# Optimization experiments

Measured on AMD Instinct MI355X. Metric: run time of the kernel, lower is better.

Reference implementation:

```python
import jax, jax.numpy as jnp
import numpy as np

B, P, K = 8, 1024, 20  # clouds, points per cloud, kNN neighbors
OUT = 40
EPS = 1e-5


def leaky(x):
    return jnp.where(x >= 0, x, 0.2 * x)


def batch_norm(h, gamma, beta):
    mu = jnp.mean(h, axis=0)
    var = jnp.var(h, axis=0)
    return (h - mu) * jax.lax.rsqrt(var + EPS) * gamma + beta


def edge_conv(x, W, b, k):
    # x: [B,P,C]. Dynamic kNN in feature space (self included, as torch_cluster knn),
    # edge feature nn([x_i, x_j - x_i]) (single plain Linear per PyG MLP plain_last),
    # then max-aggregation over the k neighbors.
    sq = jnp.sum(x * x, axis=-1)                                  # [B,P]
    d = sq[:, :, None] + sq[:, None, :] - 2.0 * jnp.einsum('bpc,bqc->bpq', x, x)
    idx = jax.lax.top_k(-d, k)[1]                                  # [B,P,k]
    xj = jax.vmap(lambda xc, ic: xc[ic])(x, idx)                   # [B,P,k,C]
    xi = jnp.broadcast_to(x[:, :, None, :], xj.shape)
    e = jnp.concatenate([xi, xj - xi], axis=-1)                    # [B,P,k,2C]
    h = jnp.einsum('bpke,ec->bpkc', e, W) + b
    return jnp.max(h, axis=2)                                      # [B,P,Cout]


def setup_inputs() -> dict:
    key = jax.random.key(0)
    ks = jax.random.split(key, 16)
    s = 0.1
    pos = jax.random.normal(ks[0], (B * P, 3), dtype=jnp.float32)
    batch = jnp.repeat(jnp.arange(B, dtype=jnp.int32), P)
    return {
        'pos': pos, 'batch': batch,
        'W1': jax.random.normal(ks[1], (6, 64), jnp.float32) * s,    'b1': jnp.zeros((64,), jnp.float32),
        'W2': jax.random.normal(ks[2], (128, 64), jnp.float32) * s,  'b2': jnp.zeros((64,), jnp.float32),
        'W3': jax.random.normal(ks[3], (128, 128), jnp.float32) * s, 'b3': jnp.zeros((128,), jnp.float32),
        'W4': jax.random.normal(ks[4], (256, 256), jnp.float32) * s, 'b4': jnp.zeros((256,), jnp.float32),
        'Wm': jax.random.normal(ks[5], (512, 1024), jnp.float32) * s, 'bm': jnp.zeros((1024,), jnp.float32),
        'Wa': jax.random.normal(ks[6], (2048, 512), jnp.float32) * s, 'ba': jnp.zeros((512,), jnp.float32),
        'ga': jnp.ones((512,), jnp.float32),  'bea': jnp.zeros((512,), jnp.float32),
        'Wb': jax.random.normal(ks[7], (512, 256), jnp.float32) * s, 'bb': jnp.zeros((256,), jnp.float32),
        'gb': jnp.ones((256,), jnp.float32),  'beb': jnp.zeros((256,), jnp.float32),
        'Wc': jax.random.normal(ks[8], (256, OUT), jnp.float32) * s, 'bc': jnp.zeros((OUT,), jnp.float32),
    }


def reference(pos, batch, W1, b1, W2, b2, W3, b3, W4, b4, Wm, bm,
              Wa, ba, ga, bea, Wb, bb, gb, beb, Wc, bc):
    # batch ids are contiguous with P points per cloud -> reshape to [B,P,.]
    x = pos.reshape(B, P, 3)
    x1 = edge_conv(x, W1, b1, K)    # [B,P,64]
    x2 = edge_conv(x1, W2, b2, K)   # [B,P,64]
    x3 = edge_conv(x2, W3, b3, K)   # [B,P,128]
    x4 = edge_conv(x3, W4, b4, K)   # [B,P,256]
    cat = jnp.concatenate([x1, x2, x3, x4], axis=-1)  # [B,P,512]
    out = cat @ Wm + bm                                # [B,P,1024] (plain Linear)
    gmax = jnp.max(out, axis=1)                        # global_max_pool  [B,1024]
    gmean = jnp.mean(out, axis=1)                      # global_mean_pool [B,1024]
    h = jnp.concatenate([gmax, gmean], axis=-1)        # [B,2048]
    h = leaky(batch_norm(h @ Wa + ba, ga, bea))        # dropout = identity (eval)
    h = leaky(batch_norm(h @ Wb + bb, gb, beb))
    return h @ Wc + bc                                 # [B,40]
```

## Files before the change

kernel.cpp:

```cpp
#include <hip/hip_runtime.h>
#include <hip/hip_bf16.h>

#define NB 8
#define NP 1024
#define NPTS (NB * NP)
#define KNN 20

using bf16x8 = __attribute__((ext_vector_type(8))) short;
using f32x4 = __attribute__((ext_vector_type(4))) float;

static __device__ __forceinline__ unsigned long long umin64(unsigned long long a,
                                                            unsigned long long b) {
    return a < b ? a : b;
}

static __device__ __forceinline__ void split_bf16(float v, unsigned short& h,
                                                  unsigned short& l) {
    __hip_bfloat16 hb = __float2bfloat16(v);
    float hf = __bfloat162float(hb);
    __hip_bfloat16 lb = __float2bfloat16(v - hf);
    h = *(unsigned short*)&hb;
    l = *(unsigned short*)&lb;
}

static __device__ __forceinline__ unsigned long long wave_bitonic_sort(
        unsigned long long v, int lane) {
#pragma unroll
    for (int k = 2; k <= 64; k <<= 1) {
#pragma unroll
        for (int j = k >> 1; j > 0; j >>= 1) {
            unsigned long long o = __shfl_xor(v, j, 64);
            bool tmin = (((lane & k) == 0) == ((lane & j) == 0));
            bool lt = v < o;
            v = (lt == tmin) ? v : o;
        }
    }
    return v;
}

static __device__ __forceinline__ void topk20_wave(unsigned long long k[16], int lane,
                                                   int* __restrict__ out) {
    for (int r = 0; r < KNN; ++r) {
        unsigned long long m = k[0];
#pragma unroll
        for (int j = 1; j < 16; ++j)
            if ((unsigned)(k[j] >> 32) < (unsigned)(m >> 32)) m = k[j];
#pragma unroll
        for (int s = 1; s < 64; s <<= 1) {
            unsigned long long o = __shfl_xor(m, s, 64);
            m = umin64(m, o);
        }
        if (lane == 0) out[r] = (int)(m & 0xffffffffu);
        if (r == KNN - 1) break;
        unsigned mlo = (unsigned)m;
#pragma unroll
        for (int j = 0; j < 16; ++j)
            if ((unsigned)k[j] == mlo) k[j] = ~0ull;
    }
}

static __device__ __forceinline__ void topk20_fast(unsigned long long k[16], int lane,
                                                   unsigned long long* __restrict__ cand,
                                                   int* __restrict__ out) {
    unsigned long long lm = k[0];
#pragma unroll
    for (int j = 1; j < 16; ++j) lm = umin64(lm, k[j]);
    unsigned long long s = wave_bitonic_sort(lm, lane);
    unsigned long long T = __shfl(s, 19, 64);

    int base = 0;
#pragma unroll
    for (int j = 0; j < 16; ++j) {
        bool sel = (k[j] <= T);
        unsigned long long mask = __ballot(sel);
        if (sel) {
            int pos = base + (int)__popcll(mask & ((1ull << lane) - 1ull));
            if (pos < 64) cand[pos] = k[j];
        }
        base += (int)__popcll(mask);
    }
    if (base <= 64) {
        unsigned long long v = (lane < base) ? cand[lane] : ~0ull;
        v = wave_bitonic_sort(v, lane);
        if (lane < KNN) out[lane] = (int)(v & 0xffffffffu);
    } else {
        topk20_wave(k, lane, out);
    }
}

__global__ __launch_bounds__(256) void knn3_kernel(const float* __restrict__ x,
                                                   int* __restrict__ idx) {
    const int w = threadIdx.x >> 6, lane = threadIdx.x & 63;
    const int p = blockIdx.x * 4 + w;
    const int b = p >> 10, pr = p & 1023;
    const int tid = threadIdx.x;
    __shared__ float sx[3][1024];
    __shared__ float ssq[1024];
    __shared__ unsigned long long cand[4][64];
    const float* xb = x + (size_t)b * NP * 3;

    for (int t = tid; t < 1024; t += 256) {
        float vx = xb[t * 3 + 0], vy = xb[t * 3 + 1], vz = xb[t * 3 + 2];
        sx[0][t] = vx;
        sx[1][t] = vy;
        sx[2][t] = vz;
        ssq[t] = vx * vx + vy * vy + vz * vz;
    }
    __syncthreads();

    const float px = sx[0][pr], py = sx[1][pr], pz = sx[2][pr];
    const float sqp = ssq[pr];

    unsigned long long k[16];
#pragma unroll
    for (int j = 0; j < 16; ++j) {
        int q = j * 64 + lane;
        float dot = px * sx[0][q];
        dot += py * sx[1][q];
        dot += pz * sx[2][q];
        float d = sqp + ssq[q] - 2.0f * dot;
        unsigned u = __float_as_uint(d);
        u = (u & 0x80000000u) ? ~u : (u | 0x80000000u);
        k[j] = ((unsigned long long)u << 32) | (unsigned)q;
    }
    topk20_fast(k, lane, cand[w], idx + (size_t)p * KNN);
}

template <int C>
__global__ __launch_bounds__(256) void sqnorm_kernel(const float* __restrict__ x,
                                                     float* __restrict__ sqn) {
    int p = blockIdx.x * 256 + threadIdx.x;
    if (p < NPTS) {
        const float* xp = x + (size_t)p * C;
        float s = 0.f;
        for (int c = 0; c < C; ++c) s += xp[c] * xp[c];
        sqn[p] = s;
    }
}

template <int C>
__global__ __launch_bounds__(256) void convert_x_kernel(const float* __restrict__ x,
                                                        unsigned short* __restrict__ Xh,
                                                        unsigned short* __restrict__ Xl) {
    int g = blockIdx.x * 256 + threadIdx.x;
    int p = g & (NPTS - 1), ks = g >> 13;
    const float* src = x + (size_t)p * C + ks * 8;
    float4 v0 = ((const float4*)src)[0];
    float4 v1 = ((const float4*)src)[1];
    float v[8] = {v0.x, v0.y, v0.z, v0.w, v1.x, v1.y, v1.z, v1.w};
    unsigned short h[8], l[8];
#pragma unroll
    for (int j = 0; j < 8; ++j) split_bf16(v[j], h[j], l[j]);
    size_t ci = (size_t)ks * NPTS + p;
    uint4 hp, lp;
    hp.x = h[0] | ((unsigned)h[1] << 16);
    hp.y = h[2] | ((unsigned)h[3] << 16);
    hp.z = h[4] | ((unsigned)h[5] << 16);
    hp.w = h[6] | ((unsigned)h[7] << 16);
    lp.x = l[0] | ((unsigned)l[1] << 16);
    lp.y = l[2] | ((unsigned)l[3] << 16);
    lp.z = l[4] | ((unsigned)l[5] << 16);
    lp.w = l[6] | ((unsigned)l[7] << 16);
    ((uint4*)Xh)[ci] = hp;
    ((uint4*)Xl)[ci] = lp;
}

template <int Cin, int Cout>
__global__ __launch_bounds__(256) void convert_w_edge_kernel(
        const float* __restrict__ W, unsigned short* __restrict__ Wh,
        unsigned short* __restrict__ Wl) {
    constexpr int N2 = 2 * Cout;
    int g = blockIdx.x * 256 + threadIdx.x;
    if (g >= (Cin / 8) * N2) return;
    int n = g % N2, ks = g / N2;
    unsigned short h[8], l[8];
#pragma unroll
    for (int j = 0; j < 8; ++j) {
        int c = ks * 8 + j;
        float v;
        if (n < Cout)
            v = W[(size_t)c * Cout + n] - W[(size_t)(Cin + c) * Cout + n];
        else
            v = W[(size_t)(Cin + c) * Cout + (n - Cout)];
        split_bf16(v, h[j], l[j]);
    }
    size_t ci = (size_t)ks * N2 + n;
    uint4 hp, lp;
    hp.x = h[0] | ((unsigned)h[1] << 16);
    hp.y = h[2] | ((unsigned)h[3] << 16);
    hp.z = h[4] | ((unsigned)h[5] << 16);
    hp.w = h[6] | ((unsigned)h[7] << 16);
    lp.x = l[0] | ((unsigned)l[1] << 16);
    lp.y = l[2] | ((unsigned)l[3] << 16);
    lp.z = l[4] | ((unsigned)l[5] << 16);
    lp.w = l[6] | ((unsigned)l[7] << 16);
    ((uint4*)Wh)[ci] = hp;
    ((uint4*)Wl)[ci] = lp;
}

template <int C>
__global__ __launch_bounds__(256, 2) void dist_mfma_kernel(
        const unsigned short* __restrict__ Xhp, const unsigned short* __restrict__ Xlp,
        const float* __restrict__ sqn, float* __restrict__ Dm) {
    constexpr int NCK = C / 32;
    const int b = blockIdx.z;
    const int p0 = blockIdx.y * 128;
    const int q0 = blockIdx.x * 128;
    const int g0 = b * NP;
    const int tid = threadIdx.x;
    const int wid = tid >> 6, lane = tid & 63;
    const int wm = (wid >> 1) * 64, wn = (wid & 1) * 64;

    __shared__ uint4 sAh[2][4][132], sAl[2][4][132], sBh[2][4][132], sBl[2][4][132];
    __shared__ float sqa[128], sqb[128];

    f32x4 acc[4][4];
#pragma unroll
    for (int i = 0; i < 4; ++i)
#pragma unroll
        for (int j = 0; j < 4; ++j) acc[i][j] = {0.f, 0.f, 0.f, 0.f};

    const uint4* Ah4 = (const uint4*)Xhp;
    const uint4* Al4 = (const uint4*)Xlp;

    const int m0 = tid & 127, kb0 = tid >> 7;
    uint4 rAh0, rAl0, rBh0, rBl0, rAh1, rAl1, rBh1, rBl1;

#define DM_LOAD(ck)                                                     \
    {                                                                   \
        int ksb = (ck) * 4;                                             \
        size_t a0 = (size_t)(ksb + kb0) * NPTS + g0 + p0 + m0;          \
        size_t a1 = (size_t)(ksb + kb0 + 2) * NPTS + g0 + p0 + m0;      \
        size_t b0 = (size_t)(ksb + kb0) * NPTS + g0 + q0 + m0;          \
        size_t b1 = (size_t)(ksb + kb0 + 2) * NPTS + g0 + q0 + m0;      \
        rAh0 = Ah4[a0]; rAl0 = Al4[a0];                                 \
        rAh1 = Ah4[a1]; rAl1 = Al4[a1];                                 \
        rBh0 = Ah4[b0]; rBl0 = Al4[b0];                                 \
        rBh1 = Ah4[b1]; rBl1 = Al4[b1];                                 \
    }

#define DM_WRITE(buf)                                                   \
    {                                                                   \
        sAh[buf][kb0][m0] = rAh0;  sAl[buf][kb0][m0] = rAl0;            \
        sAh[buf][kb0 + 2][m0] = rAh1;  sAl[buf][kb0 + 2][m0] = rAl1;    \
        sBh[buf][kb0][m0] = rBh0;  sBl[buf][kb0][m0] = rBl0;            \
        sBh[buf][kb0 + 2][m0] = rBh1;  sBl[buf][kb0 + 2][m0] = rBl1;    \
    }

    DM_LOAD(0);
    DM_WRITE(0);
    __syncthreads();

    const int fkb = lane >> 4, flm = lane & 15;

    for (int ck = 0; ck < NCK; ++ck) {
        const int buf = ck & 1;
        if (ck < NCK - 1) DM_LOAD(ck + 1);

        bf16x8 fAh[4], fAl[4], fBh[4], fBl[4];
#pragma unroll
        for (int i = 0; i < 4; ++i) {
            fAh[i] = *(const bf16x8*)&sAh[buf][fkb][wm + i * 16 + flm];
            fAl[i] = *(const bf16x8*)&sAl[buf][fkb][wm + i * 16 + flm];
            fBh[i] = *(const bf16x8*)&sBh[buf][fkb][wn + i * 16 + flm];
            fBl[i] = *(const bf16x8*)&sBl[buf][fkb][wn + i * 16 + flm];
        }
#pragma unroll
        for (int i = 0; i < 4; ++i)
#pragma unroll
            for (int j = 0; j < 4; ++j) {
                acc[i][j] = __builtin_amdgcn_mfma_f32_16x16x32_bf16(fAh[i], fBh[j],
                                                                    acc[i][j], 0, 0, 0);
                acc[i][j] = __builtin_amdgcn_mfma_f32_16x16x32_bf16(fAh[i], fBl[j],
                                                                    acc[i][j], 0, 0, 0);
                acc[i][j] = __builtin_amdgcn_mfma_f32_16x16x32_bf16(fAl[i], fBh[j],
                                                                    acc[i][j], 0, 0, 0);
            }

        if (ck < NCK - 1) DM_WRITE(buf ^ 1);
        __syncthreads();
    }

    if (tid < 128) sqa[tid] = sqn[g0 + p0 + tid];
    else sqb[tid - 128] = sqn[g0 + q0 + (tid - 128)];
    __syncthreads();

    const int r4 = (lane >> 4) * 4, cc = lane & 15;
#pragma unroll
    for (int i = 0; i < 4; ++i) {
#pragma unroll
        for (int r = 0; r < 4; ++r) {
            int row = wm + i * 16 + r4 + r;
            float sp = sqa[row];
            float* drow = Dm + ((size_t)(g0 + p0 + row)) * NP + q0;
#pragma unroll
            for (int j = 0; j < 4; ++j) {
                int col = wn + j * 16 + cc;
                drow[col] = sp + sqb[col] - 2.0f * acc[i][j][r];
            }
        }
    }
#undef DM_LOAD
#undef DM_WRITE
}

template <int Cin, int Cout>
__global__ __launch_bounds__(256, 2) void edge_mfma_kernel(
        const unsigned short* __restrict__ Xhp, const unsigned short* __restrict__ Xlp,
        const unsigned short* __restrict__ Whp, const unsigned short* __restrict__ Wlp,
        const float* __restrict__ bias, float* __restrict__ AB) {
    constexpr int N2 = 2 * Cout;
    constexpr int NCK = Cin / 32;
    const int n0 = blockIdx.x * 128;
    const int p0 = blockIdx.y * 128;
    const int tid = threadIdx.x;
    const int wid = tid >> 6, lane = tid & 63;
    const int wm = (wid >> 1) * 64, wn = (wid & 1) * 64;

    __shared__ uint4 sAh[2][4][132], sAl[2][4][132], sBh[2][4][132], sBl[2][4][132];

    f32x4 acc[4][4];
#pragma unroll
    for (int i = 0; i < 4; ++i)
#pragma unroll
        for (int j = 0; j < 4; ++j) acc[i][j] = {0.f, 0.f, 0.f, 0.f};

    const uint4* Ah4 = (const uint4*)Xhp;
    const uint4* Al4 = (const uint4*)Xlp;
    const uint4* Wh4 = (const uint4*)Whp;
    const uint4* Wl4 = (const uint4*)Wlp;

    const int m0 = tid & 127, kb0 = tid >> 7;
    uint4 rAh0, rAl0, rBh0, rBl0, rAh1, rAl1, rBh1, rBl1;

#define EM_LOAD(ck)                                                     \
    {                                                                   \
        int ksb = (ck) * 4;                                             \
        size_t a0 = (size_t)(ksb + kb0) * NPTS + p0 + m0;               \
        size_t a1 = (size_t)(ksb + kb0 + 2) * NPTS + p0 + m0;           \
        size_t b0 = (size_t)(ksb + kb0) * N2 + n0 + m0;                 \
        size_t b1 = (size_t)(ksb + kb0 + 2) * N2 + n0 + m0;             \
        rAh0 = Ah4[a0]; rAl0 = Al4[a0];                                 \
        rAh1 = Ah4[a1]; rAl1 = Al4[a1];                                 \
        rBh0 = Wh4[b0]; rBl0 = Wl4[b0];                                 \
        rBh1 = Wh4[b1]; rBl1 = Wl4[b1];                                 \
    }

#define EM_WRITE(buf)                                                   \
    {                                                                   \
        sAh[buf][kb0][m0] = rAh0;  sAl[buf][kb0][m0] = rAl0;            \
        sAh[buf][kb0 + 2][m0] = rAh1;  sAl[buf][kb0 + 2][m0] = rAl1;    \
        sBh[buf][kb0][m0] = rBh0;  sBl[buf][kb0][m0] = rBl0;            \
        sBh[buf][kb0 + 2][m0] = rBh1;  sBl[buf][kb0 + 2][m0] = rBl1;    \
    }

    EM_LOAD(0);
    EM_WRITE(0);
    __syncthreads();

    const int fkb = lane >> 4, flm = lane & 15;

    for (int ck = 0; ck < NCK; ++ck) {
        const int buf = ck & 1;
        if (ck < NCK - 1) EM_LOAD(ck + 1);

        bf16x8 fAh[4], fAl[4], fBh[4], fBl[4];
#pragma unroll
        for (int i = 0; i < 4; ++i) {
            fAh[i] = *(const bf16x8*)&sAh[buf][fkb][wm + i * 16 + flm];
            fAl[i] = *(const bf16x8*)&sAl[buf][fkb][wm + i * 16 + flm];
            fBh[i] = *(const bf16x8*)&sBh[buf][fkb][wn + i * 16 + flm];
            fBl[i] = *(const bf16x8*)&sBl[buf][fkb][wn + i * 16 + flm];
        }
#pragma unroll
        for (int i = 0; i < 4; ++i)
#pragma unroll
            for (int j = 0; j < 4; ++j) {
                acc[i][j] = __builtin_amdgcn_mfma_f32_16x16x32_bf16(fAh[i], fBh[j],
                                                                    acc[i][j], 0, 0, 0);
                acc[i][j] = __builtin_amdgcn_mfma_f32_16x16x32_bf16(fAh[i], fBl[j],
                                                                    acc[i][j], 0, 0, 0);
                acc[i][j] = __builtin_amdgcn_mfma_f32_16x16x32_bf16(fAl[i], fBh[j],
                                                                    acc[i][j], 0, 0, 0);
            }

        if (ck < NCK - 1) EM_WRITE(buf ^ 1);
        __syncthreads();
    }

    const int r4 = (lane >> 4) * 4, cc = lane & 15;
    float bj[4];
#pragma unroll
    for (int j = 0; j < 4; ++j) {
        int cg = n0 + wn + j * 16 + cc;
        bj[j] = (cg < Cout) ? bias[cg] : 0.f;
    }
#pragma unroll
    for (int i = 0; i < 4; ++i) {
#pragma unroll
        for (int r = 0; r < 4; ++r) {
            int row = wm + i * 16 + r4 + r;
            float* orow = AB + (size_t)(p0 + row) * N2 + n0;
#pragma unroll
            for (int j = 0; j < 4; ++j)
                orow[wn + j * 16 + cc] = acc[i][j][r] + bj[j];
        }
    }
#undef EM_LOAD
#undef EM_WRITE
}

__global__ __launch_bounds__(256) void topk_kernel(const float* __restrict__ Dm,
                                                   int* __restrict__ idx) {
    const int w = threadIdx.x >> 6, lane = threadIdx.x & 63;
    const int p = blockIdx.x * 4 + w;
    const int b = p >> 10, pr = p & 1023;
    const float* row = Dm + ((size_t)b * NP + pr) * NP;
    __shared__ unsigned long long cand[4][64];

    unsigned long long k[16];
#pragma unroll
    for (int j = 0; j < 16; ++j) {
        int q = j * 64 + lane;
        float dv = row[q];
        unsigned u = __float_as_uint(dv);
        u = (u & 0x80000000u) ? ~u : (u | 0x80000000u);
        k[j] = ((unsigned long long)u << 32) | (unsigned)q;
    }
    topk20_fast(k, lane, cand[w], idx + (size_t)p * KNN);
}

template <int Cin, int Cout>
__global__ __launch_bounds__(256) void edge_gemm_kernel(const float* __restrict__ x,
                                                        const float* __restrict__ W,
                                                        const float* __restrict__ bias,
                                                        float* __restrict__ AB) {
    constexpr int N2 = 2 * Cout;
    constexpr int BK = (Cin < 32) ? Cin : 32;
    const int n0 = blockIdx.x * 128;
    const int p0 = blockIdx.y * 64;
    const int tid = threadIdx.x;
    const int tx = tid & 15, ty = tid >> 4;

    __shared__ float sX[BK][68];
    __shared__ float sW[BK][132];

    float acc[4][8];
#pragma unroll
    for (int i = 0; i < 4; ++i)
#pragma unroll
        for (int j = 0; j < 8; ++j) acc[i][j] = 0.f;

    for (int k0 = 0; k0 < Cin; k0 += BK) {
        for (int t = tid; t < 64 * BK; t += 256) {
            int m = t / BK, c = t - m * BK;
            sX[c][m] = x[(size_t)(p0 + m) * Cin + c];
        }
        for (int t = tid; t < BK * 128; t += 256) {
            int c = t >> 7, n = t & 127;
            int nn = n0 + n;
            float w;
            if (nn < Cout)
                w = W[(size_t)(k0 + c) * Cout + nn] - W[(size_t)(Cin + k0 + c) * Cout + nn];
            else
                w = W[(size_t)(Cin + k0 + c) * Cout + (nn - Cout)];
            sW[c][n] = w;
        }
        __syncthreads();

#pragma unroll
        for (int c = 0; c < BK; ++c) {
            float4 a4 = *(const float4*)&sX[c][ty * 4];
            float4 w0 = *(const float4*)&sW[c][tx * 4];
            float4 w1 = *(const float4*)&sW[c][64 + tx * 4];
            float av[4] = {a4.x, a4.y, a4.z, a4.w};
#pragma unroll
            for (int i = 0; i < 4; ++i) {
                acc[i][0] += av[i] * w0.x;
                acc[i][1] += av[i] * w0.y;
                acc[i][2] += av[i] * w0.z;
                acc[i][3] += av[i] * w0.w;
                acc[i][4] += av[i] * w1.x;
                acc[i][5] += av[i] * w1.y;
                acc[i][6] += av[i] * w1.z;
                acc[i][7] += av[i] * w1.w;
            }
        }
        __syncthreads();
    }

    const bool aH0 = (n0 < Cout);
    const bool aH1 = (n0 + 64 < Cout);
    float4 z4 = {0.f, 0.f, 0.f, 0.f};
    float4 bb0 = aH0 ? *(const float4*)&bias[n0 + tx * 4] : z4;
    float4 bb1 = aH1 ? *(const float4*)&bias[n0 + 64 + tx * 4] : z4;

#pragma unroll
    for (int i = 0; i < 4; ++i) {
        float* orow = AB + (size_t)(p0 + ty * 4 + i) * N2 + n0;
        float4 o0, o1;
        o0.x = acc[i][0] + bb0.x;
        o0.y = acc[i][1] + bb0.y;
        o0.z = acc[i][2] + bb0.z;
        o0.w = acc[i][3] + bb0.w;
        o1.x = acc[i][4] + bb1.x;
        o1.y = acc[i][5] + bb1.y;
        o1.z = acc[i][6] + bb1.z;
        o1.w = acc[i][7] + bb1.w;
        *(float4*)&orow[tx * 4] = o0;
        *(float4*)&orow[64 + tx * 4] = o1;
    }
}

template <int Cout>
__global__ __launch_bounds__(256) void gather_max_kernel(const float* __restrict__ AB,
                                                         const int* __restrict__ idx,
                                                         float* __restrict__ y) {
    constexpr int N2 = 2 * Cout;
    constexpr int TPP = Cout / 4;
    constexpr int PPB = 256 / TPP;
    constexpr int RS = N2 / 4;
    const int pp = threadIdx.x / TPP;
    const int t = threadIdx.x % TPP;
    const int p = blockIdx.x * PPB + pp;
    const int base = p & ~(NP - 1);

    __shared__ int s_idx[PPB][KNN];
    for (int tt = threadIdx.x; tt < PPB * KNN; tt += 256) {
        int a = tt / KNN, r = tt - a * KNN;
        s_idx[a][r] = idx[(size_t)(blockIdx.x * PPB + a) * KNN + r];
    }
    __syncthreads();

    const float4* Brow = (const float4*)(AB + (size_t)base * N2 + Cout);

    int q0 = s_idx[pp][0];
    float4 m = Brow[(size_t)q0 * RS + t];
#pragma unroll
    for (int j = 1; j < KNN; ++j) {
        int q = s_idx[pp][j];
        float4 v = Brow[(size_t)q * RS + t];
        m.x = fmaxf(m.x, v.x);
        m.y = fmaxf(m.y, v.y);
        m.z = fmaxf(m.z, v.z);
        m.w = fmaxf(m.w, v.w);
    }
    float4 a = *(const float4*)(AB + (size_t)p * N2 + 4 * t);
    float4 o;
    o.x = a.x + m.x;
    o.y = a.y + m.y;
    o.z = a.z + m.z;
    o.w = a.w + m.w;
    *(float4*)(y + (size_t)p * Cout + 4 * t) = o;
}

__global__ __launch_bounds__(256) void convert_w_kernel(const float* __restrict__ Wm,
                                                        unsigned short* __restrict__ Wh,
                                                        unsigned short* __restrict__ Wl) {
    int g = blockIdx.x * 256 + threadIdx.x;
    int n = g & 1023, ks = g >> 10;
    unsigned short h[8], l[8];
#pragma unroll
    for (int j = 0; j < 8; ++j) {
        float v = Wm[(size_t)(ks * 8 + j) * 1024 + n];
        split_bf16(v, h[j], l[j]);
    }
    size_t ci = (size_t)ks * 1024 + n;
    uint4 hp, lp;
    hp.x = h[0] | ((unsigned)h[1] << 16);
    hp.y = h[2] | ((unsigned)h[3] << 16);
    hp.z = h[4] | ((unsigned)h[5] << 16);
    hp.w = h[6] | ((unsigned)h[7] << 16);
    lp.x = l[0] | ((unsigned)l[1] << 16);
    lp.y = l[2] | ((unsigned)l[3] << 16);
    lp.z = l[4] | ((unsigned)l[5] << 16);
    lp.w = l[6] | ((unsigned)l[7] << 16);
    ((uint4*)Wh)[ci] = hp;
    ((uint4*)Wl)[ci] = lp;
}

__global__ __launch_bounds__(256) void catmean_kernel(
        const float* __restrict__ x1, const float* __restrict__ x2,
        const float* __restrict__ x3, const float* __restrict__ x4,
        float* __restrict__ catmean) {
    const int n0 = blockIdx.x * 128;
    const int b = blockIdx.y;
    const int tid = threadIdx.x;
    const int col = n0 + (tid & 127);
    const int half = tid >> 7;
    __shared__ float sred[256];

    const float* src;
    int cw, coff;
    if (col < 64) { src = x1; cw = 64; coff = col; }
    else if (col < 128) { src = x2; cw = 64; coff = col - 64; }
    else if (col < 256) { src = x3; cw = 128; coff = col - 128; }
    else { src = x4; cw = 256; coff = col - 256; }

    float s = 0.f;
    const float* base = src + ((size_t)b * NP + half * 512) * cw + coff;
    for (int p = 0; p < 512; ++p) s += base[(size_t)p * cw];
    sred[tid] = s;
    __syncthreads();
    if (tid < 128)
        catmean[(size_t)b * 512 + col] = (sred[tid] + sred[tid + 128]) * (1.0f / 1024.0f);
}

__global__ __launch_bounds__(256) void gmean_kernel(const float* __restrict__ catmean,
                                                    const float* __restrict__ Wm,
                                                    const float* __restrict__ bm,
                                                    float* __restrict__ gmeanv) {
    const int n0 = blockIdx.x * 128;
    const int b = blockIdx.y;
    const int tid = threadIdx.x;
    const int cg = tid & 31, kp = tid >> 5;
    const int col = n0 + cg * 4;
    __shared__ float4 part[8][32];

    float4 acc = {0.f, 0.f, 0.f, 0.f};
    for (int k = kp * 64; k < kp * 64 + 64; ++k) {
        float g = catmean[(size_t)b * 512 + k];
        float4 w = *(const float4*)&Wm[(size_t)k * 1024 + col];
        acc.x += g * w.x;
        acc.y += g * w.y;
        acc.z += g * w.z;
        acc.w += g * w.w;
    }
    part[kp][cg] = acc;
    __syncthreads();
    if (tid < 32) {
        float4 s = part[0][tid];
#pragma unroll
        for (int z = 1; z < 8; ++z) {
            float4 p = part[z][tid];
            s.x += p.x; s.y += p.y; s.z += p.z; s.w += p.w;
        }
        float4 bb = *(const float4*)&bm[n0 + tid * 4];
        s.x += bb.x; s.y += bb.y; s.z += bb.z; s.w += bb.w;
        *(float4*)&gmeanv[(size_t)b * 1024 + n0 + tid * 4] = s;
    }
}

__global__ __launch_bounds__(256, 2) void gemm_cat_pool_kernel(
        const unsigned short* __restrict__ Ahp, const unsigned short* __restrict__ Alp,
        const unsigned short* __restrict__ Whp, const unsigned short* __restrict__ Wlp,
        float* __restrict__ pmax) {
    const int bid = blockIdx.x;
    const int xcd = bid & 7, pos = bid >> 3;
    const int nb = pos & 7, pb = (xcd << 3) | (pos >> 3);
    const int n0 = nb * 128, p0 = pb * 128;
    const int tid = threadIdx.x;
    const int wid = tid >> 6, lane = tid & 63;
    const int wm = (wid >> 1) * 64, wn = (wid & 1) * 64;

    __shared__ uint4 sAh[2][4][132], sAl[2][4][132], sBh[2][4][132], sBl[2][4][132];
    __shared__ float sMax[2][128];

    f32x4 acc[4][4];
#pragma unroll
    for (int i = 0; i < 4; ++i)
#pragma unroll
        for (int j = 0; j < 4; ++j) acc[i][j] = {0.f, 0.f, 0.f, 0.f};

    const uint4* Ah4 = (const uint4*)Ahp;
    const uint4* Al4 = (const uint4*)Alp;
    const uint4* Wh4 = (const uint4*)Whp;
    const uint4* Wl4 = (const uint4*)Wlp;

    const int m0 = tid & 127, kb0 = tid >> 7;
    uint4 rAh0, rAl0, rBh0, rBl0, rAh1, rAl1, rBh1, rBl1;

#define MP_LOAD(ck)                                                     \
    {                                                                   \
        int ksb = (ck) * 4;                                             \
        size_t a0 = (size_t)(ksb + kb0) * 8192 + p0 + m0;               \
        size_t a1 = (size_t)(ksb + kb0 + 2) * 8192 + p0 + m0;           \
        size_t b0 = (size_t)(ksb + kb0) * 1024 + n0 + m0;               \
        size_t b1 = (size_t)(ksb + kb0 + 2) * 1024 + n0 + m0;           \
        rAh0 = Ah4[a0]; rAl0 = Al4[a0];                                 \
        rAh1 = Ah4[a1]; rAl1 = Al4[a1];                                 \
        rBh0 = Wh4[b0]; rBl0 = Wl4[b0];                                 \
        rBh1 = Wh4[b1]; rBl1 = Wl4[b1];                                 \
    }

#define MP_WRITE(buf)                                                   \
    {                                                                   \
        sAh[buf][kb0][m0] = rAh0;  sAl[buf][kb0][m0] = rAl0;            \
        sAh[buf][kb0 + 2][m0] = rAh1;  sAl[buf][kb0 + 2][m0] = rAl1;    \
        sBh[buf][kb0][m0] = rBh0;  sBl[buf][kb0][m0] = rBl0;            \
        sBh[buf][kb0 + 2][m0] = rBh1;  sBl[buf][kb0 + 2][m0] = rBl1;    \
    }

    MP_LOAD(0);
    MP_WRITE(0);
    __syncthreads();

    const int fkb = lane >> 4, flm = lane & 15;

    for (int ck = 0; ck < 16; ++ck) {
        const int buf = ck & 1;
        if (ck < 15) MP_LOAD(ck + 1);

        bf16x8 fAh[4], fAl[4], fBh[4], fBl[4];
#pragma unroll
        for (int i = 0; i < 4; ++i) {
            fAh[i] = *(const bf16x8*)&sAh[buf][fkb][wm + i * 16 + flm];
            fAl[i] = *(const bf16x8*)&sAl[buf][fkb][wm + i * 16 + flm];
            fBh[i] = *(const bf16x8*)&sBh[buf][fkb][wn + i * 16 + flm];
            fBl[i] = *(const bf16x8*)&sBl[buf][fkb][wn + i * 16 + flm];
        }
#pragma unroll
        for (int i = 0; i < 4; ++i)
#pragma unroll
            for (int j = 0; j < 4; ++j) {
                acc[i][j] = __builtin_amdgcn_mfma_f32_16x16x32_bf16(fAh[i], fBh[j],
                                                                    acc[i][j], 0, 0, 0);
                acc[i][j] = __builtin_amdgcn_mfma_f32_16x16x32_bf16(fAh[i], fBl[j],
                                                                    acc[i][j], 0, 0, 0);
                acc[i][j] = __builtin_amdgcn_mfma_f32_16x16x32_bf16(fAl[i], fBh[j],
                                                                    acc[i][j], 0, 0, 0);
            }

        if (ck < 15) MP_WRITE(buf ^ 1);
        __syncthreads();
    }

    float cm[4];
#pragma unroll
    for (int j = 0; j < 4; ++j) {
        float m = acc[0][j][0];
#pragma unroll
        for (int i = 0; i < 4; ++i)
#pragma unroll
            for (int r = 0; r < 4; ++r) m = fmaxf(m, acc[i][j][r]);
        m = fmaxf(m, __shfl_xor(m, 16, 64));
        m = fmaxf(m, __shfl_xor(m, 32, 64));
        cm[j] = m;
    }
    if (lane < 16) {
#pragma unroll
        for (int j = 0; j < 4; ++j) sMax[wid >> 1][wn + j * 16 + lane] = cm[j];
    }
    __syncthreads();
    if (tid < 128)
        pmax[(size_t)pb * 1024 + n0 + tid] = fmaxf(sMax[0][tid], sMax[1][tid]);
#undef MP_LOAD
#undef MP_WRITE
}

__global__ __launch_bounds__(256) void fc_a_kernel(const float* __restrict__ pmax,
                                                   const float* __restrict__ gmeanv,
                                                   const float* __restrict__ bm,
                                                   const float* __restrict__ Wa,
                                                   const float* __restrict__ ba,
                                                   float* __restrict__ ha) {
    const int b = blockIdx.y;
    const int n0 = blockIdx.x * 64;
    const int tid = threadIdx.x;
    __shared__ float gm[2048];
    __shared__ float4 part[16][16];

    for (int c = tid; c < 1024; c += 256) {
        float m = pmax[(size_t)(b * 8) * 1024 + c];
#pragma unroll
        for (int z = 1; z < 8; ++z) m = fmaxf(m, pmax[(size_t)(b * 8 + z) * 1024 + c]);
        gm[c] = m + bm[c];
        gm[1024 + c] = gmeanv[(size_t)b * 1024 + c];
    }
    __syncthreads();

    const int cg = tid & 15, kp = tid >> 4;
    const int co = n0 + cg * 4;
    float4 acc = {0.f, 0.f, 0.f, 0.f};
    const float* Wp = Wa + (size_t)(kp * 128) * 512 + co;
    const float* gp = gm + kp * 128;
#pragma unroll 8
    for (int k = 0; k < 128; ++k) {
        float g = gp[k];
        float4 w = *(const float4*)&Wp[(size_t)k * 512];
        acc.x += g * w.x;
        acc.y += g * w.y;
        acc.z += g * w.z;
        acc.w += g * w.w;
    }
    part[kp][cg] = acc;
    __syncthreads();
    if (tid < 16) {
        float4 s = part[0][tid];
#pragma unroll
        for (int z = 1; z < 16; ++z) {
            float4 p = part[z][tid];
            s.x += p.x; s.y += p.y; s.z += p.z; s.w += p.w;
        }
        float4 bb = *(const float4*)&ba[n0 + tid * 4];
        s.x += bb.x; s.y += bb.y; s.z += bb.z; s.w += bb.w;
        *(float4*)&ha[(size_t)b * 512 + n0 + tid * 4] = s;
    }
}

__global__ __launch_bounds__(256) void bn_leaky_kernel(float* __restrict__ h,
                                                       const float* __restrict__ g,
                                                       const float* __restrict__ be,
                                                       int ncol) {
    int co = blockIdx.x * 256 + threadIdx.x;
    if (co >= ncol) return;
    float mu = 0.f;
    for (int b = 0; b < NB; ++b) mu += h[b * ncol + co];
    mu *= 0.125f;
    float var = 0.f;
    for (int b = 0; b < NB; ++b) {
        float d = h[b * ncol + co] - mu;
        var += d * d;
    }
    var *= 0.125f;
    float inv = 1.0f / sqrtf(var + 1e-5f);
    for (int b = 0; b < NB; ++b) {
        float v = (h[b * ncol + co] - mu) * inv * g[co] + be[co];
        h[b * ncol + co] = v >= 0.f ? v : 0.2f * v;
    }
}

__global__ __launch_bounds__(256) void fc_b_kernel(const float* __restrict__ ha,
                                                   const float* __restrict__ Wb,
                                                   const float* __restrict__ bb,
                                                   float* __restrict__ hb) {
    const int b = blockIdx.y;
    const int n0 = blockIdx.x * 64;
    const int tid = threadIdx.x;
    __shared__ float sh[512];
    __shared__ float4 part[16][16];

    for (int c = tid; c < 512; c += 256) sh[c] = ha[(size_t)b * 512 + c];
    __syncthreads();

    const int cg = tid & 15, kp = tid >> 4;
    const int co = n0 + cg * 4;
    float4 acc = {0.f, 0.f, 0.f, 0.f};
#pragma unroll 8
    for (int k = 0; k < 32; ++k) {
        float g = sh[kp * 32 + k];
        float4 w = *(const float4*)&Wb[(size_t)(kp * 32 + k) * 256 + co];
        acc.x += g * w.x;
        acc.y += g * w.y;
        acc.z += g * w.z;
        acc.w += g * w.w;
    }
    part[kp][cg] = acc;
    __syncthreads();
    if (tid < 16) {
        float4 s = part[0][tid];
#pragma unroll
        for (int z = 1; z < 16; ++z) {
            float4 p = part[z][tid];
            s.x += p.x; s.y += p.y; s.z += p.z; s.w += p.w;
        }
        float4 bv = *(const float4*)&bb[n0 + tid * 4];
        s.x += bv.x; s.y += bv.y; s.z += bv.z; s.w += bv.w;
        *(float4*)&hb[(size_t)b * 256 + n0 + tid * 4] = s;
    }
}

__global__ __launch_bounds__(256) void fc_c_kernel(const float* __restrict__ hb,
                                                   const float* __restrict__ Wc,
                                                   const float* __restrict__ bc,
                                                   float* __restrict__ outp) {
    int t = blockIdx.x * 256 + threadIdx.x;
    if (t >= 8 * 40) return;
    int b = t / 40, o = t - b * 40;
    float s = bc[o];
    for (int c = 0; c < 256; ++c) s += hb[b * 256 + c] * Wc[c * 40 + o];
    outp[t] = s;
}

extern "C" void kernel_launch(void* const* d_in, const int* in_sizes, int n_in,
                              void* d_out, int out_size, void* d_ws, size_t ws_size,
                              hipStream_t stream) {
    const float* pos = (const float*)d_in[0];
    const float* W1 = (const float*)d_in[2];
    const float* b1 = (const float*)d_in[3];
    const float* W2 = (const float*)d_in[4];
    const float* b2 = (const float*)d_in[5];
    const float* W3 = (const float*)d_in[6];
    const float* b3 = (const float*)d_in[7];
    const float* W4 = (const float*)d_in[8];
    const float* b4 = (const float*)d_in[9];
    const float* Wm = (const float*)d_in[10];
    const float* bm = (const float*)d_in[11];
    const float* Wa = (const float*)d_in[12];
    const float* ba = (const float*)d_in[13];
    const float* ga = (const float*)d_in[14];
    const float* bea = (const float*)d_in[15];
    const float* Wb = (const float*)d_in[16];
    const float* bb = (const float*)d_in[17];
    const float* gb = (const float*)d_in[18];
    const float* beb = (const float*)d_in[19];
    const float* Wc = (const float*)d_in[20];
    const float* bc = (const float*)d_in[21];
    float* out = (float*)d_out;

    char* ws = (char*)d_ws;
    size_t off = 0;
    auto alloc = [&](size_t bytes) {
        void* p = ws + off;
        off += (bytes + 255) & ~(size_t)255;
        return p;
    };
    int* idx = (int*)alloc((size_t)NPTS * KNN * 4);
    float* x1 = (float*)alloc((size_t)NPTS * 64 * 4);
    float* x2 = (float*)alloc((size_t)NPTS * 64 * 4);
    float* x3 = (float*)alloc((size_t)NPTS * 128 * 4);
    float* x4 = (float*)alloc((size_t)NPTS * 256 * 4);
    float* scratch = (float*)alloc((size_t)NPTS * 1024 * 4);
    float* pmax = (float*)alloc((size_t)64 * 1024 * 4);
    float* catmean = (float*)alloc(NB * 512 * 4);
    float* gmeanv = (float*)alloc(NB * 1024 * 4);
    float* ha = (float*)alloc(NB * 512 * 4);
    float* hb = (float*)alloc(NB * 256 * 4);
    float* sqn = (float*)alloc(NPTS * 4);
    unsigned short* Ach = (unsigned short*)alloc((size_t)64 * NPTS * 8 * 2);
    unsigned short* Acl = (unsigned short*)alloc((size_t)64 * NPTS * 8 * 2);
    unsigned short* Wth = (unsigned short*)alloc((size_t)64 * 1024 * 8 * 2);
    unsigned short* Wtl = (unsigned short*)alloc((size_t)64 * 1024 * 8 * 2);
    unsigned short* Weh = (unsigned short*)alloc((size_t)16 * 512 * 8 * 2);
    unsigned short* Wel = (unsigned short*)alloc((size_t)16 * 512 * 8 * 2);
    (void)ws_size;

    float* Dm = scratch;
    float* AB = scratch;
    const size_t REG = (size_t)NPTS * 8;
    unsigned short* x1h = Ach, *x1l = Acl;
    unsigned short* x2h = Ach + 8 * REG, *x2l = Acl + 8 * REG;
    unsigned short* x3h = Ach + 16 * REG, *x3l = Acl + 16 * REG;
    unsigned short* x4h = Ach + 32 * REG, *x4l = Acl + 32 * REG;

    dim3 dmg(8, 8, 8);

    knn3_kernel<<<NPTS / 4, 256, 0, stream>>>(pos, idx);
    edge_gemm_kernel<3, 64><<<dim3(1, 128), 256, 0, stream>>>(pos, W1, b1, AB);
    gather_max_kernel<64><<<NPTS / 16, 256, 0, stream>>>(AB, idx, x1);

    convert_x_kernel<64><<<NPTS * 8 / 256, 256, 0, stream>>>(x1, x1h, x1l);
    sqnorm_kernel<64><<<NPTS / 256, 256, 0, stream>>>(x1, sqn);
    dist_mfma_kernel<64><<<dmg, 256, 0, stream>>>(x1h, x1l, sqn, Dm);
    topk_kernel<<<NPTS / 4, 256, 0, stream>>>(Dm, idx);
    convert_w_edge_kernel<64, 64><<<4, 256, 0, stream>>>(W2, Weh, Wel);
    edge_mfma_kernel<64, 64><<<dim3(1, 64), 256, 0, stream>>>(x1h, x1l, Weh, Wel, b2, AB);
    gather_max_kernel<64><<<NPTS / 16, 256, 0, stream>>>(AB, idx, x2);

    convert_x_kernel<64><<<NPTS * 8 / 256, 256, 0, stream>>>(x2, x2h, x2l);
    sqnorm_kernel<64><<<NPTS / 256, 256, 0, stream>>>(x2, sqn);
    dist_mfma_kernel<64><<<dmg, 256, 0, stream>>>(x2h, x2l, sqn, Dm);
    topk_kernel<<<NPTS / 4, 256, 0, stream>>>(Dm, idx);
    convert_w_edge_kernel<64, 128><<<8, 256, 0, stream>>>(W3, Weh, Wel);
    edge_mfma_kernel<64, 128><<<dim3(2, 64), 256, 0, stream>>>(x2h, x2l, Weh, Wel, b3, AB);
    gather_max_kernel<128><<<NPTS / 8, 256, 0, stream>>>(AB, idx, x3);

    convert_x_kernel<128><<<NPTS * 16 / 256, 256, 0, stream>>>(x3, x3h, x3l);
    sqnorm_kernel<128><<<NPTS / 256, 256, 0, stream>>>(x3, sqn);
    dist_mfma_kernel<128><<<dmg, 256, 0, stream>>>(x3h, x3l, sqn, Dm);
    topk_kernel<<<NPTS / 4, 256, 0, stream>>>(Dm, idx);
    convert_w_edge_kernel<128, 256><<<32, 256, 0, stream>>>(W4, Weh, Wel);
    edge_mfma_kernel<128, 256><<<dim3(4, 64), 256, 0, stream>>>(x3h, x3l, Weh, Wel, b4, AB);
    gather_max_kernel<256><<<NPTS / 4, 256, 0, stream>>>(AB, idx, x4);

    convert_x_kernel<256><<<NPTS * 32 / 256, 256, 0, stream>>>(x4, x4h, x4l);

    catmean_kernel<<<dim3(4, NB), 256, 0, stream>>>(x1, x2, x3, x4, catmean);
    gmean_kernel<<<dim3(8, NB), 256, 0, stream>>>(catmean, Wm, bm, gmeanv);

    convert_w_kernel<<<256, 256, 0, stream>>>(Wm, Wth, Wtl);

    gemm_cat_pool_kernel<<<512, 256, 0, stream>>>(Ach, Acl, Wth, Wtl, pmax);

    fc_a_kernel<<<dim3(8, NB), 256, 0, stream>>>(pmax, gmeanv, bm, Wa, ba, ha);
    bn_leaky_kernel<<<2, 256, 0, stream>>>(ha, ga, bea, 512);
    fc_b_kernel<<<dim3(4, NB), 256, 0, stream>>>(ha, Wb, bb, hb);
    bn_leaky_kernel<<<1, 256, 0, stream>>>(hb, gb, beb, 256);
    fc_c_kernel<<<2, 256, 0, stream>>>(hb, Wc, bc, out);
}
```

Baseline: 269.2 us.

## Fuse distance GEMM and top-k selection into one kNN kernel via shared memory

Replaces the separate distance-matrix MFMA kernel and top-k kernel with one fused kernel. Each block computes a 16-row slab of the 1024-column distance matrix into LDS and runs top-20 selection per row directly, so the 32 MB distance matrix never goes to global memory. The scratch buffer shrinks to match. In exchange, B operands are loaded from global without LDS staging, each block re-reads the whole cloud's features, and the large LDS footprint (~66KB) limits occupancy.

```diff
diff --git a/kernel.cpp b/kernel.cpp
--- a/kernel.cpp
+++ b/kernel.cpp
@@ -199,109 +199,95 @@
 }
 
 template <int C>
-__global__ __launch_bounds__(256, 2) void dist_mfma_kernel(
+__global__ __launch_bounds__(256, 2) void knn_mfma_kernel(
         const unsigned short* __restrict__ Xhp, const unsigned short* __restrict__ Xlp,
-        const float* __restrict__ sqn, float* __restrict__ Dm) {
+        const float* __restrict__ sqn, int* __restrict__ idx) {
     constexpr int NCK = C / 32;
-    const int b = blockIdx.z;
-    const int p0 = blockIdx.y * 128;
-    const int q0 = blockIdx.x * 128;
+    const int bid = blockIdx.x;
+    const int b = bid >> 6, rg = bid & 63;
     const int g0 = b * NP;
+    const int p0 = rg * 16;
     const int tid = threadIdx.x;
     const int wid = tid >> 6, lane = tid & 63;
-    const int wm = (wid >> 1) * 64, wn = (wid & 1) * 64;
-
-    __shared__ uint4 sAh[2][4][132], sAl[2][4][132], sBh[2][4][132], sBl[2][4][132];
-    __shared__ float sqa[128], sqb[128];
-
-    f32x4 acc[4][4];
-#pragma unroll
-    for (int i = 0; i < 4; ++i)
-#pragma unroll
-        for (int j = 0; j < 4; ++j) acc[i][j] = {0.f, 0.f, 0.f, 0.f};
+    const int fkb = lane >> 4, flm = lane & 15;
+
+    __shared__ float sD[16][1028];
+    __shared__ float sqa[16];
+    __shared__ float sqb[1024];
+    __shared__ unsigned long long cand[4][64];
+
+    if (tid < 16) sqa[tid] = sqn[g0 + p0 + tid];
+    for (int t = tid; t < 1024; t += 256) sqb[t] = sqn[g0 + t];
+    __syncthreads();
 
     const uint4* Ah4 = (const uint4*)Xhp;
     const uint4* Al4 = (const uint4*)Xlp;
 
-    const int m0 = tid & 127, kb0 = tid >> 7;
-    uint4 rAh0, rAl0, rBh0, rBl0, rAh1, rAl1, rBh1, rBl1;
-
-#define DM_LOAD(ck)                                                     \
-    {                                                                   \
-        int ksb = (ck) * 4;                                             \
-        size_t a0 = (size_t)(ksb + kb0) * NPTS + g0 + p0 + m0;          \
-        size_t a1 = (size_t)(ksb + kb0 + 2) * NPTS + g0 + p0 + m0;      \
-        size_t b0 = (size_t)(ksb + kb0) * NPTS + g0 + q0 + m0;          \
-        size_t b1 = (size_t)(ksb + kb0 + 2) * NPTS + g0 + q0 + m0;      \
-        rAh0 = Ah4[a0]; rAl0 = Al4[a0];                                 \
-        rAh1 = Ah4[a1]; rAl1 = Al4[a1];                                 \
-        rBh0 = Ah4[b0]; rBl0 = Al4[b0];                                 \
-        rBh1 = Ah4[b1]; rBl1 = Al4[b1];                                 \
-    }
-
-#define DM_WRITE(buf)                                                   \
-    {                                                                   \
-        sAh[buf][kb0][m0] = rAh0;  sAl[buf][kb0][m0] = rAl0;            \
-        sAh[buf][kb0 + 2][m0] = rAh1;  sAl[buf][kb0 + 2][m0] = rAl1;    \
-        sBh[buf][kb0][m0] = rBh0;  sBl[buf][kb0][m0] = rBl0;            \
-        sBh[buf][kb0 + 2][m0] = rBh1;  sBl[buf][kb0 + 2][m0] = rBl1;    \
-    }
-
-    DM_LOAD(0);
-    DM_WRITE(0);
-    __syncthreads();
-
-    const int fkb = lane >> 4, flm = lane & 15;
-
-    for (int ck = 0; ck < NCK; ++ck) {
-        const int buf = ck & 1;
-        if (ck < NCK - 1) DM_LOAD(ck + 1);
-
-        bf16x8 fAh[4], fAl[4], fBh[4], fBl[4];
-#pragma unroll
-        for (int i = 0; i < 4; ++i) {
-            fAh[i] = *(const bf16x8*)&sAh[buf][fkb][wm + i * 16 + flm];
-            fAl[i] = *(const bf16x8*)&sAl[buf][fkb][wm + i * 16 + flm];
-            fBh[i] = *(const bf16x8*)&sBh[buf][fkb][wn + i * 16 + flm];
-            fBl[i] = *(const bf16x8*)&sBl[buf][fkb][wn + i * 16 + flm];
-        }
-#pragma unroll
-        for (int i = 0; i < 4; ++i)
-#pragma unroll
-            for (int j = 0; j < 4; ++j) {
-                acc[i][j] = __builtin_amdgcn_mfma_f32_16x16x32_bf16(fAh[i], fBh[j],
-                                                                    acc[i][j], 0, 0, 0);
-                acc[i][j] = __builtin_amdgcn_mfma_f32_16x16x32_bf16(fAh[i], fBl[j],
-                                                                    acc[i][j], 0, 0, 0);
-                acc[i][j] = __builtin_amdgcn_mfma_f32_16x16x32_bf16(fAl[i], fBh[j],
-                                                                    acc[i][j], 0, 0, 0);
+    uint4 fAh[NCK], fAl[NCK];
+#pragma unroll
+    for (int kk = 0; kk < NCK; ++kk) {
+        size_t a = (size_t)(4 * kk + fkb) * NPTS + g0 + p0 + flm;
+        fAh[kk] = Ah4[a];
+        fAl[kk] = Al4[a];
+    }
+
+    const int r4 = fkb * 4, cc = flm;
+
+#pragma unroll
+    for (int t = 0; t < 2; ++t) {
+        const int c0 = (wid + t * 4) * 128;
+        f32x4 acc[8];
+#pragma unroll
+        for (int j = 0; j < 8; ++j) acc[j] = {0.f, 0.f, 0.f, 0.f};
+
+#pragma unroll
+        for (int kk = 0; kk < NCK; ++kk) {
+            uint4 fBh[8], fBl[8];
+#pragma unroll
+            for (int j = 0; j < 8; ++j) {
+                size_t bi = (size_t)(4 * kk + fkb) * NPTS + g0 + c0 + j * 16 + flm;
+                fBh[j] = Ah4[bi];
+                fBl[j] = Al4[bi];
             }
-
-        if (ck < NCK - 1) DM_WRITE(buf ^ 1);
-        __syncthreads();
-    }
-
-    if (tid < 128) sqa[tid] = sqn[g0 + p0 + tid];
-    else sqb[tid - 128] = sqn[g0 + q0 + (tid - 128)];
-    __syncthreads();
-
-    const int r4 = (lane >> 4) * 4, cc = lane & 15;
-#pragma unroll
-    for (int i = 0; i < 4; ++i) {
+            bf16x8 ah = *(const bf16x8*)&fAh[kk];
+            bf16x8 al = *(const bf16x8*)&fAl[kk];
+#pragma unroll
+            for (int j = 0; j < 8; ++j) {
+                bf16x8 bh = *(const bf16x8*)&fBh[j];
+                bf16x8 bl = *(const bf16x8*)&fBl[j];
+                acc[j] = __builtin_amdgcn_mfma_f32_16x16x32_bf16(ah, bh, acc[j], 0, 0, 0);
+                acc[j] = __builtin_amdgcn_mfma_f32_16x16x32_bf16(ah, bl, acc[j], 0, 0, 0);
+                acc[j] = __builtin_amdgcn_mfma_f32_16x16x32_bf16(al, bh, acc[j], 0, 0, 0);
+            }
+        }
+
 #pragma unroll
         for (int r = 0; r < 4; ++r) {
-            int row = wm + i * 16 + r4 + r;
+            int row = r4 + r;
             float sp = sqa[row];
-            float* drow = Dm + ((size_t)(g0 + p0 + row)) * NP + q0;
-#pragma unroll
-            for (int j = 0; j < 4; ++j) {
-                int col = wn + j * 16 + cc;
-                drow[col] = sp + sqb[col] - 2.0f * acc[i][j][r];
+#pragma unroll
+            for (int j = 0; j < 8; ++j) {
+                int col = c0 + j * 16 + cc;
+                sD[row][col] = sp + sqb[col] - 2.0f * acc[j][r];
             }
         }
     }
-#undef DM_LOAD
-#undef DM_WRITE
+    __syncthreads();
+
+    for (int rr = 0; rr < 4; ++rr) {
+        int row = wid * 4 + rr;
+        unsigned long long k[16];
+#pragma unroll
+        for (int j = 0; j < 16; ++j) {
+            int q = j * 64 + lane;
+            float dv = sD[row][q];
+            unsigned u = __float_as_uint(dv);
+            u = (u & 0x80000000u) ? ~u : (u | 0x80000000u);
+            k[j] = ((unsigned long long)u << 32) | (unsigned)q;
+        }
+        topk20_fast(k, lane, cand[wid], idx + (size_t)(g0 + p0 + row) * KNN);
+        __builtin_amdgcn_s_barrier();
+    }
 }
 
 template <int Cin, int Cout>
@@ -408,26 +394,6 @@
     }
 #undef EM_LOAD
 #undef EM_WRITE
-}
-
-__global__ __launch_bounds__(256) void topk_kernel(const float* __restrict__ Dm,
-                                                   int* __restrict__ idx) {
-    const int w = threadIdx.x >> 6, lane = threadIdx.x & 63;
-    const int p = blockIdx.x * 4 + w;
-    const int b = p >> 10, pr = p & 1023;
-    const float* row = Dm + ((size_t)b * NP + pr) * NP;
-    __shared__ unsigned long long cand[4][64];
-
-    unsigned long long k[16];
-#pragma unroll
-    for (int j = 0; j < 16; ++j) {
-        int q = j * 64 + lane;
-        float dv = row[q];
-        unsigned u = __float_as_uint(dv);
-        u = (u & 0x80000000u) ? ~u : (u | 0x80000000u);
-        k[j] = ((unsigned long long)u << 32) | (unsigned)q;
-    }
-    topk20_fast(k, lane, cand[w], idx + (size_t)p * KNN);
 }
 
 template <int Cin, int Cout>
@@ -910,7 +876,7 @@
     float* x2 = (float*)alloc((size_t)NPTS * 64 * 4);
     float* x3 = (float*)alloc((size_t)NPTS * 128 * 4);
     float* x4 = (float*)alloc((size_t)NPTS * 256 * 4);
-    float* scratch = (float*)alloc((size_t)NPTS * 1024 * 4);
+    float* scratch = (float*)alloc((size_t)NPTS * 512 * 4);
     float* pmax = (float*)alloc((size_t)64 * 1024 * 4);
     float* catmean = (float*)alloc(NB * 512 * 4);
     float* gmeanv = (float*)alloc(NB * 1024 * 4);
@@ -925,7 +891,6 @@
     unsigned short* Wel = (unsigned short*)alloc((size_t)16 * 512 * 8 * 2);
     (void)ws_size;
 
-    float* Dm = scratch;
     float* AB = scratch;
     const size_t REG = (size_t)NPTS * 8;
     unsigned short* x1h = Ach, *x1l = Acl;
@@ -933,32 +898,27 @@
     unsigned short* x3h = Ach + 16 * REG, *x3l = Acl + 16 * REG;
     unsigned short* x4h = Ach + 32 * REG, *x4l = Acl + 32 * REG;
 
-    dim3 dmg(8, 8, 8);
-
     knn3_kernel<<<NPTS / 4, 256, 0, stream>>>(pos, idx);
     edge_gemm_kernel<3, 64><<<dim3(1, 128), 256, 0, stream>>>(pos, W1, b1, AB);
     gather_max_kernel<64><<<NPTS / 16, 256, 0, stream>>>(AB, idx, x1);
 
     convert_x_kernel<64><<<NPTS * 8 / 256, 256, 0, stream>>>(x1, x1h, x1l);
     sqnorm_kernel<64><<<NPTS / 256, 256, 0, stream>>>(x1, sqn);
-    dist_mfma_kernel<64><<<dmg, 256, 0, stream>>>(x1h, x1l, sqn, Dm);
-    topk_kernel<<<NPTS / 4, 256, 0, stream>>>(Dm, idx);
+    knn_mfma_kernel<64><<<512, 256, 0, stream>>>(x1h, x1l, sqn, idx);
     convert_w_edge_kernel<64, 64><<<4, 256, 0, stream>>>(W2, Weh, Wel);
     edge_mfma_kernel<64, 64><<<dim3(1, 64), 256, 0, stream>>>(x1h, x1l, Weh, Wel, b2, AB);
     gather_max_kernel<64><<<NPTS / 16, 256, 0, stream>>>(AB, idx, x2);
 
     convert_x_kernel<64><<<NPTS * 8 / 256, 256, 0, stream>>>(x2, x2h, x2l);
     sqnorm_kernel<64><<<NPTS / 256, 256, 0, stream>>>(x2, sqn);
-    dist_mfma_kernel<64><<<dmg, 256, 0, stream>>>(x2h, x2l, sqn, Dm);
-    topk_kernel<<<NPTS / 4, 256, 0, stream>>>(Dm, idx);
+    knn_mfma_kernel<64><<<512, 256, 0, stream>>>(x2h, x2l, sqn, idx);
     convert_w_edge_kernel<64, 128><<<8, 256, 0, stream>>>(W3, Weh, Wel);
     edge_mfma_kernel<64, 128><<<dim3(2, 64), 256, 0, stream>>>(x2h, x2l, Weh, Wel, b3, AB);
     gather_max_kernel<128><<<NPTS / 8, 256, 0, stream>>>(AB, idx, x3);
 
     convert_x_kernel<128><<<NPTS * 16 / 256, 256, 0, stream>>>(x3, x3h, x3l);
     sqnorm_kernel<128><<<NPTS / 256, 256, 0, stream>>>(x3, sqn);
-    dist_mfma_kernel<128><<<dmg, 256, 0, stream>>>(x3h, x3l, sqn, Dm);
-    topk_kernel<<<NPTS / 4, 256, 0, stream>>>(Dm, idx);
+    knn_mfma_kernel<128><<<512, 256, 0, stream>>>(x3h, x3l, sqn, idx);
     convert_w_edge_kernel<128, 256><<<32, 256, 0, stream>>>(W4, Weh, Wel);
     edge_mfma_kernel<128, 256><<<dim3(4, 64), 256, 0, stream>>>(x3h, x3l, Weh, Wel, b4, AB);
     gather_max_kernel<256><<<NPTS / 4, 256, 0, stream>>>(AB, idx, x4);
```

New measurement: 268.9 us. Within noise of the previous version (-0.1%).
